# Kernel optimization log

Hardware: AMD Instinct MI355X
Metric: run time of the kernel (lower is better)

## Reference

```python
import jax, jax.numpy as jnp
import numpy as np

NUM_EMBEDDINGS = 4096
EMBEDDING_DIM = 256
COMMITMENT_COST = 0.25


def setup_inputs() -> dict:
    key = jax.random.key(0)
    k1, k2 = jax.random.split(key)
    z = jax.random.normal(k1, (16, 4096, EMBEDDING_DIM), dtype=jnp.float32)
    # nn.Embedding init: uniform(-1/K, 1/K)
    emb_w = jax.random.uniform(
        k2, (NUM_EMBEDDINGS, EMBEDDING_DIM), dtype=jnp.float32,
        minval=-1.0 / NUM_EMBEDDINGS, maxval=1.0 / NUM_EMBEDDINGS)
    return {"z": z, "emb_w": emb_w}


def reference(z, emb_w):
    B = z.shape[0]
    D = emb_w.shape[1]
    flat_z = z.reshape(-1, D)  # [T, D]
    # squared L2 distances: ||z||^2 - 2 z.E^T + ||e||^2  -> [T, K]
    distances = (jnp.sum(flat_z ** 2, axis=1, keepdims=True)
                 - 2.0 * flat_z @ emb_w.T
                 + jnp.sum(emb_w ** 2, axis=1))
    encoding_indices = jnp.argmin(distances, axis=1)  # [T]
    quantized = emb_w[encoding_indices]  # [T, D]
    # straight-through estimator
    quantized = flat_z + jax.lax.stop_gradient(quantized - flat_z)
    loss = (jnp.mean((jax.lax.stop_gradient(quantized) - flat_z) ** 2)
            + COMMITMENT_COST * jnp.mean((quantized - jax.lax.stop_gradient(flat_z)) ** 2))
    return (quantized.reshape(z.shape),
            encoding_indices.reshape(B, -1),
            loss)
```

## Files before the change

### kernel.cpp

```cpp
#include <hip/hip_runtime.h>
#include <cfloat>
#include <climits>

#define T_TOKENS 65536
#define K_EMB 4096
#define D_DIM 256
#define QOFF ((size_t)T_TOKENS * D_DIM)
#define WINDOW 1.2e-4f
#define B0 0.03125f

using bf16x8 = __attribute__((ext_vector_type(8))) short;
using f32x16 = __attribute__((ext_vector_type(16))) float;

__device__ __forceinline__ float fmul_nc(float a, float b) {
    float c = a * b;
    asm volatile("" : "+v"(c));
    return c;
}

__device__ __forceinline__ double wave_sum_d(double v) {
#pragma unroll
    for (int o = 32; o >= 1; o >>= 1) v += __shfl_down(v, o, 64);
    return v;
}

__device__ __forceinline__ void glds16(const void* g, void* l) {
    __builtin_amdgcn_global_load_lds((const __attribute__((address_space(1))) void*)g,
                                     (__attribute__((address_space(3))) void*)l, 16, 0, 0);
}

__device__ __forceinline__ unsigned short f2bf(float f) {
    unsigned u = __float_as_uint(f);
    u += 0x7FFFu + ((u >> 16) & 1u);
    return (unsigned short)(u >> 16);
}

__global__ __launch_bounds__(256)
void a32_kernel(const float* __restrict__ z, float* __restrict__ a32) {
    __shared__ float lds[64][257];
    const int tid = threadIdx.x;
    const int t0 = blockIdx.x * 256;
    for (int sub = 0; sub < 4; sub++) {
        const int tb = t0 + sub * 64;
        __syncthreads();
        for (int idx = tid; idx < 64 * 256; idx += 256) {
            const int r = idx >> 8, c = idx & 255;
            lds[r][c] = z[(size_t)(tb + r) * D_DIM + c];
        }
        __syncthreads();
        if (tid < 64) {
            const float* row = lds[tid];
            float S[2];
            for (int h = 0; h < 2; h++) {
                const float* p = row + h * 128;
                float r[8];
#pragma unroll
                for (int j = 0; j < 8; j++) r[j] = fmul_nc(p[j], p[j]);
                for (int m = 1; m < 16; m++) {
#pragma unroll
                    for (int j = 0; j < 8; j++) r[j] += fmul_nc(p[8 * m + j], p[8 * m + j]);
                }
                S[h] = ((r[0] + r[1]) + (r[2] + r[3])) + ((r[4] + r[5]) + (r[6] + r[7]));
            }
            a32[tb + tid] = S[0] + S[1];
        }
    }
}

__global__ void c32_kernel(const float* __restrict__ emb, float* __restrict__ c32) {
    const int k = blockIdx.x;
    const double v = (double)emb[(size_t)k * D_DIM + threadIdx.x];
    double s = wave_sum_d(v * v);
    __shared__ double wsm[4];
    const int lane = threadIdx.x & 63, w = threadIdx.x >> 6;
    if (lane == 0) wsm[w] = s;
    __syncthreads();
    if (threadIdx.x == 0) c32[k] = (float)(wsm[0] + wsm[1] + wsm[2] + wsm[3]);
}

__global__ __launch_bounds__(256)
void split_hi_kernel(const float* __restrict__ emb, unsigned short* __restrict__ ehi) {
    const size_t i4 = (size_t)blockIdx.x * 256 + threadIdx.x;
    const float4 v = *(const float4*)(emb + i4 * 4);
    ushort4 hh;
    hh.x = f2bf(v.x); hh.y = f2bf(v.y); hh.z = f2bf(v.z); hh.w = f2bf(v.w);
    *(ushort4*)(ehi + i4 * 4) = hh;
}

__global__ __launch_bounds__(256, 4)
void argmin_mfma_kernel(const float* __restrict__ z,
                        const unsigned short* __restrict__ ehi,
                        unsigned int* __restrict__ keyout)
{
    __shared__ short lds_e[2][32 * 256];

    const int tid = threadIdx.x;
    const int wv  = tid >> 6;
    const int l   = tid & 63;
    const int lr  = l & 31;
    const int h   = l >> 5;
    const int tok = blockIdx.x * 128 + wv * 32 + lr;
    const int kbase = blockIdx.y * 2048;

    bf16x8 zh[16];
#pragma unroll
    for (int st = 0; st < 16; st++) {
        const float* zp = z + (size_t)tok * D_DIM + st * 16 + h * 8;
        const float4 f0 = *(const float4*)zp;
        const float4 f1 = *(const float4*)(zp + 4);
        const float f[8] = {f0.x, f0.y, f0.z, f0.w, f1.x, f1.y, f1.z, f1.w};
#pragma unroll
        for (int j = 0; j < 8; j++) zh[st][j] = (short)f2bf(f[j]);
    }

    unsigned b1 = 0u, b2 = 0u, b3 = 0u, b4 = 0u;

    auto stage = [&](int buf, int ct) {
#pragma unroll
        for (int q = 0; q < 4; q++) {
            const int rp = wv * 4 + q;
            const int r  = 2 * rp + h;
            const int g  = lr ^ ((2 * q) | h);
            const unsigned short* src =
                ehi + (size_t)(kbase + ct * 32 + r) * D_DIM + g * 8;
            glds16(src, &lds_e[buf][rp * 512]);
        }
    };

    stage(0, 0);
    __syncthreads();

    const int lk = lr & 7;
    const short* lrow0 = &lds_e[0][lr * 256];
    const short* lrow1 = &lds_e[1][lr * 256];
    const unsigned vh4 = (unsigned)(4 * h);

    int buf = 0;
    for (int ct = 0; ct < 64; ct++) {
        if (ct + 1 < 64) stage(buf ^ 1, ct + 1);

        f32x16 aP;
#pragma unroll
        for (int i = 0; i < 16; i++) aP[i] = B0;

        const short* lrow = buf ? lrow1 : lrow0;
#pragma unroll
        for (int st = 0; st < 16; st++) {
            const bf16x8 eh = *(const bf16x8*)(lrow + (((2 * st + h) ^ lk) << 3));
            aP = __builtin_amdgcn_mfma_f32_32x32x16_bf16(eh, zh[st], aP, 0, 0, 0);
        }

        const unsigned korb = (unsigned)(kbase + ct * 32) | vh4;
#pragma unroll
        for (int r = 0; r < 16; r++) {
            const float cv = fmaxf(aP[r], 1e-6f);
            unsigned t = (__float_as_uint(cv) & 0xFFFFF000u) | korb
                         | (unsigned)((r & 3) + 8 * (r >> 2));
            const unsigned n1 = b1 > t ? b1 : t; t = b1 > t ? t : b1; b1 = n1;
            const unsigned n2 = b2 > t ? b2 : t; t = b2 > t ? t : b2; b2 = n2;
            const unsigned n3 = b3 > t ? b3 : t; t = b3 > t ? t : b3; b3 = n3;
            b4 = b4 > t ? b4 : t;
        }
        __syncthreads();
        buf ^= 1;
    }

    *(uint4*)(keyout + (((size_t)blockIdx.y * T_TOKENS + tok) << 3) + vh4) =
        make_uint4(b1, b2, b3, b4);
}

__global__ __launch_bounds__(256)
void rescore_gather_kernel(const float* __restrict__ z, const float* __restrict__ emb,
                           const float* __restrict__ a32, const float* __restrict__ c32,
                           const unsigned int* __restrict__ keyout,
                           float* __restrict__ out, double* __restrict__ partials)
{
    __shared__ float zt[64][257];
    __shared__ int win[64];
    __shared__ double lsm[4];
    const int tid = threadIdx.x;
    const int base = blockIdx.x * 64;

    for (int idx = tid; idx < 64 * 256; idx += 256) {
        const int r = idx >> 8, c = idx & 255;
        zt[r][c] = z[(size_t)(base + r) * D_DIM + c];
    }
    __syncthreads();

    if (tid < 64) {
        const int t = base + tid;
        unsigned keys[16];
        const uint4 k0 = *(const uint4*)(keyout + ((size_t)t << 3));
        const uint4 k1 = *(const uint4*)(keyout + ((size_t)t << 3) + 4);
        const uint4 k2 = *(const uint4*)(keyout + ((size_t)(T_TOKENS + t) << 3));
        const uint4 k3 = *(const uint4*)(keyout + ((size_t)(T_TOKENS + t) << 3) + 4);
        keys[0] = k0.x; keys[1] = k0.y; keys[2] = k0.z; keys[3] = k0.w;
        keys[4] = k1.x; keys[5] = k1.y; keys[6] = k1.z; keys[7] = k1.w;
        keys[8] = k2.x; keys[9] = k2.y; keys[10] = k2.z; keys[11] = k2.w;
        keys[12] = k3.x; keys[13] = k3.y; keys[14] = k3.z; keys[15] = k3.w;
        float maxF = 0.0f;
#pragma unroll
        for (int s = 0; s < 16; s++) maxF = fmaxf(maxF, __uint_as_float(keys[s]));
        const float thr = maxF - WINDOW;
        const float ar = a32[t];
        float bestv = FLT_MAX; int bestk = INT_MAX;
        for (int s = 0; s < 16; s++) {
            if (__uint_as_float(keys[s]) >= thr) {
                const int k = (int)(keys[s] & 0xFFFu);
                const float* er = emb + (size_t)k * D_DIM;
                float m = 0.0f;
#pragma unroll 8
                for (int d4 = 0; d4 < 64; d4++) {
                    const float4 e4 = *(const float4*)(er + 4 * d4);
                    m = fmaf(zt[tid][4 * d4 + 0], e4.x, m);
                    m = fmaf(zt[tid][4 * d4 + 1], e4.y, m);
                    m = fmaf(zt[tid][4 * d4 + 2], e4.z, m);
                    m = fmaf(zt[tid][4 * d4 + 3], e4.w, m);
                }
                const float v1 = ar - 2.0f * m;
                const float v2 = v1 + c32[k];
                if (v2 < bestv || (v2 == bestv && k < bestk)) { bestv = v2; bestk = k; }
            }
        }
        win[tid] = bestk;
    }
    __syncthreads();

    double lacc = 0.0;
    for (int ti = 0; ti < 64; ti++) {
        const int sel = win[ti];
        const float ev = emb[(size_t)sel * D_DIM + tid];
        const float zv = zt[ti][tid];
        out[(size_t)(base + ti) * D_DIM + tid] = ev;
        if (tid == 0) out[QOFF + base + ti] = (float)sel;
        const double df = (double)zv - (double)ev;
        lacc += df * df;
    }
    lacc = wave_sum_d(lacc);
    const int lane = tid & 63, w = tid >> 6;
    if (lane == 0) lsm[w] = lacc;
    __syncthreads();
    if (tid == 0) partials[blockIdx.x] = lsm[0] + lsm[1] + lsm[2] + lsm[3];
}

__global__ void finalize_kernel(const double* __restrict__ partials, float* __restrict__ out) {
    __shared__ double rsm[4];
    const int tid = threadIdx.x;
    double s = 0.0;
    for (int i = tid; i < 1024; i += 256) s += partials[i];
    s = wave_sum_d(s);
    if ((tid & 63) == 0) rsm[tid >> 6] = s;
    __syncthreads();
    if (tid == 0) {
        const double mean = (rsm[0] + rsm[1] + rsm[2] + rsm[3]) / (double)QOFF;
        out[QOFF + T_TOKENS] = (float)(1.25 * mean);
    }
}

extern "C" void kernel_launch(void* const* d_in, const int* in_sizes, int n_in,
                              void* d_out, int out_size, void* d_ws, size_t ws_size,
                              hipStream_t stream)
{
    const float* z = (const float*)d_in[0];
    const float* emb = (const float*)d_in[1];
    float* out = (float*)d_out;
    char* ws = (char*)d_ws;

    float* a32 = (float*)ws;
    float* c32 = (float*)(ws + 262144);
    unsigned int* keyout = (unsigned int*)(ws + 278528);
    unsigned short* ehi = (unsigned short*)(ws + 4472832);
    double* partials = (double*)(ws + 6569984);

    split_hi_kernel<<<1024, 256, 0, stream>>>(emb, ehi);
    a32_kernel<<<T_TOKENS / 256, 256, 0, stream>>>(z, a32);
    c32_kernel<<<K_EMB, 256, 0, stream>>>(emb, c32);
    argmin_mfma_kernel<<<dim3(T_TOKENS / 128, 2), 256, 0, stream>>>(z, ehi, keyout);
    rescore_gather_kernel<<<T_TOKENS / 64, 256, 0, stream>>>(z, emb, a32, c32, keyout, out, partials);
    finalize_kernel<<<1, 256, 0, stream>>>(partials, out);
}
```

Baseline: 462.0 us.

## Fuse prep kernels, double tokens per wave in argmin, parallelize rescore

Merges the bf16 split and codebook-norm kernels into one pass and folds the token-norm computation into the rescore kernel, cutting kernel launches and an extra read of z. The MFMA argmin kernel now processes two 32-token groups per wave, so each LDS codebook fragment feeds two MFMAs and the codebook is streamed half as many times. It also drops the 4-waves-per-SIMD launch bound, and register pressure rises. Rescore now spreads candidate evaluation over all 256 threads with a shared-memory reduction instead of 64 threads doing serial work. The fmaxf clamp on scores is also removed.

```diff
diff --git a/kernel.cpp b/kernel.cpp
--- a/kernel.cpp
+++ b/kernel.cpp
@@ -36,40 +36,12 @@
 }
 
 __global__ __launch_bounds__(256)
-void a32_kernel(const float* __restrict__ z, float* __restrict__ a32) {
-    __shared__ float lds[64][257];
-    const int tid = threadIdx.x;
-    const int t0 = blockIdx.x * 256;
-    for (int sub = 0; sub < 4; sub++) {
-        const int tb = t0 + sub * 64;
-        __syncthreads();
-        for (int idx = tid; idx < 64 * 256; idx += 256) {
-            const int r = idx >> 8, c = idx & 255;
-            lds[r][c] = z[(size_t)(tb + r) * D_DIM + c];
-        }
-        __syncthreads();
-        if (tid < 64) {
-            const float* row = lds[tid];
-            float S[2];
-            for (int h = 0; h < 2; h++) {
-                const float* p = row + h * 128;
-                float r[8];
-#pragma unroll
-                for (int j = 0; j < 8; j++) r[j] = fmul_nc(p[j], p[j]);
-                for (int m = 1; m < 16; m++) {
-#pragma unroll
-                    for (int j = 0; j < 8; j++) r[j] += fmul_nc(p[8 * m + j], p[8 * m + j]);
-                }
-                S[h] = ((r[0] + r[1]) + (r[2] + r[3])) + ((r[4] + r[5]) + (r[6] + r[7]));
-            }
-            a32[tb + tid] = S[0] + S[1];
-        }
-    }
-}
-
-__global__ void c32_kernel(const float* __restrict__ emb, float* __restrict__ c32) {
+void emb_prep_kernel(const float* __restrict__ emb, float* __restrict__ c32,
+                     unsigned short* __restrict__ ehi) {
     const int k = blockIdx.x;
-    const double v = (double)emb[(size_t)k * D_DIM + threadIdx.x];
+    const float e = emb[(size_t)k * D_DIM + threadIdx.x];
+    ehi[(size_t)k * D_DIM + threadIdx.x] = f2bf(e);
+    const double v = (double)e;
     double s = wave_sum_d(v * v);
     __shared__ double wsm[4];
     const int lane = threadIdx.x & 63, w = threadIdx.x >> 6;
@@ -79,15 +51,6 @@
 }
 
 __global__ __launch_bounds__(256)
-void split_hi_kernel(const float* __restrict__ emb, unsigned short* __restrict__ ehi) {
-    const size_t i4 = (size_t)blockIdx.x * 256 + threadIdx.x;
-    const float4 v = *(const float4*)(emb + i4 * 4);
-    ushort4 hh;
-    hh.x = f2bf(v.x); hh.y = f2bf(v.y); hh.z = f2bf(v.z); hh.w = f2bf(v.w);
-    *(ushort4*)(ehi + i4 * 4) = hh;
-}
-
-__global__ __launch_bounds__(256, 4)
 void argmin_mfma_kernel(const float* __restrict__ z,
                         const unsigned short* __restrict__ ehi,
                         unsigned int* __restrict__ keyout)
@@ -99,21 +62,33 @@
     const int l   = tid & 63;
     const int lr  = l & 31;
     const int h   = l >> 5;
-    const int tok = blockIdx.x * 128 + wv * 32 + lr;
+    const int tokA = blockIdx.x * 256 + wv * 64 + lr;
+    const int tokB = tokA + 32;
     const int kbase = blockIdx.y * 2048;
 
-    bf16x8 zh[16];
+    bf16x8 zA[16], zB[16];
 #pragma unroll
     for (int st = 0; st < 16; st++) {
-        const float* zp = z + (size_t)tok * D_DIM + st * 16 + h * 8;
-        const float4 f0 = *(const float4*)zp;
-        const float4 f1 = *(const float4*)(zp + 4);
-        const float f[8] = {f0.x, f0.y, f0.z, f0.w, f1.x, f1.y, f1.z, f1.w};
-#pragma unroll
-        for (int j = 0; j < 8; j++) zh[st][j] = (short)f2bf(f[j]);
-    }
-
-    unsigned b1 = 0u, b2 = 0u, b3 = 0u, b4 = 0u;
+        {
+            const float* zp = z + (size_t)tokA * D_DIM + st * 16 + h * 8;
+            const float4 f0 = *(const float4*)zp;
+            const float4 f1 = *(const float4*)(zp + 4);
+            const float f[8] = {f0.x, f0.y, f0.z, f0.w, f1.x, f1.y, f1.z, f1.w};
+#pragma unroll
+            for (int j = 0; j < 8; j++) zA[st][j] = (short)f2bf(f[j]);
+        }
+        {
+            const float* zp = z + (size_t)tokB * D_DIM + st * 16 + h * 8;
+            const float4 f0 = *(const float4*)zp;
+            const float4 f1 = *(const float4*)(zp + 4);
+            const float f[8] = {f0.x, f0.y, f0.z, f0.w, f1.x, f1.y, f1.z, f1.w};
+#pragma unroll
+            for (int j = 0; j < 8; j++) zB[st][j] = (short)f2bf(f[j]);
+        }
+    }
+
+    unsigned a1 = 0u, a2 = 0u, a3 = 0u, a4 = 0u;
+    unsigned c1 = 0u, c2 = 0u, c3 = 0u, c4 = 0u;
 
     auto stage = [&](int buf, int ct) {
 #pragma unroll
@@ -139,43 +114,58 @@
     for (int ct = 0; ct < 64; ct++) {
         if (ct + 1 < 64) stage(buf ^ 1, ct + 1);
 
-        f32x16 aP;
-#pragma unroll
-        for (int i = 0; i < 16; i++) aP[i] = B0;
+        f32x16 pA, pB;
+#pragma unroll
+        for (int i = 0; i < 16; i++) { pA[i] = B0; pB[i] = B0; }
 
         const short* lrow = buf ? lrow1 : lrow0;
 #pragma unroll
         for (int st = 0; st < 16; st++) {
             const bf16x8 eh = *(const bf16x8*)(lrow + (((2 * st + h) ^ lk) << 3));
-            aP = __builtin_amdgcn_mfma_f32_32x32x16_bf16(eh, zh[st], aP, 0, 0, 0);
+            pA = __builtin_amdgcn_mfma_f32_32x32x16_bf16(eh, zA[st], pA, 0, 0, 0);
+            pB = __builtin_amdgcn_mfma_f32_32x32x16_bf16(eh, zB[st], pB, 0, 0, 0);
         }
 
         const unsigned korb = (unsigned)(kbase + ct * 32) | vh4;
 #pragma unroll
         for (int r = 0; r < 16; r++) {
-            const float cv = fmaxf(aP[r], 1e-6f);
-            unsigned t = (__float_as_uint(cv) & 0xFFFFF000u) | korb
-                         | (unsigned)((r & 3) + 8 * (r >> 2));
-            const unsigned n1 = b1 > t ? b1 : t; t = b1 > t ? t : b1; b1 = n1;
-            const unsigned n2 = b2 > t ? b2 : t; t = b2 > t ? t : b2; b2 = n2;
-            const unsigned n3 = b3 > t ? b3 : t; t = b3 > t ? t : b3; b3 = n3;
-            b4 = b4 > t ? b4 : t;
+            const unsigned rid = korb | (unsigned)((r & 3) + 8 * (r >> 2));
+            unsigned t = (__float_as_uint(pA[r]) & 0xFFFFF000u) | rid;
+            {
+                const unsigned n1 = a1 > t ? a1 : t; t = a1 > t ? t : a1; a1 = n1;
+                const unsigned n2 = a2 > t ? a2 : t; t = a2 > t ? t : a2; a2 = n2;
+                const unsigned n3 = a3 > t ? a3 : t; t = a3 > t ? t : a3; a3 = n3;
+                a4 = a4 > t ? a4 : t;
+            }
+            unsigned u = (__float_as_uint(pB[r]) & 0xFFFFF000u) | rid;
+            {
+                const unsigned n1 = c1 > u ? c1 : u; u = c1 > u ? u : c1; c1 = n1;
+                const unsigned n2 = c2 > u ? c2 : u; u = c2 > u ? u : c2; c2 = n2;
+                const unsigned n3 = c3 > u ? c3 : u; u = c3 > u ? u : c3; c3 = n3;
+                c4 = c4 > u ? c4 : u;
+            }
         }
         __syncthreads();
         buf ^= 1;
     }
 
-    *(uint4*)(keyout + (((size_t)blockIdx.y * T_TOKENS + tok) << 3) + vh4) =
-        make_uint4(b1, b2, b3, b4);
+    *(uint4*)(keyout + (((size_t)blockIdx.y * T_TOKENS + tokA) << 3) + vh4) =
+        make_uint4(a1, a2, a3, a4);
+    *(uint4*)(keyout + (((size_t)blockIdx.y * T_TOKENS + tokB) << 3) + vh4) =
+        make_uint4(c1, c2, c3, c4);
 }
 
 __global__ __launch_bounds__(256)
 void rescore_gather_kernel(const float* __restrict__ z, const float* __restrict__ emb,
-                           const float* __restrict__ a32, const float* __restrict__ c32,
+                           const float* __restrict__ c32,
                            const unsigned int* __restrict__ keyout,
                            float* __restrict__ out, double* __restrict__ partials)
 {
     __shared__ float zt[64][257];
+    __shared__ float a32sm[64];
+    __shared__ unsigned lmax[4][64];
+    __shared__ float bvq[4][64];
+    __shared__ int bkq[4][64];
     __shared__ int win[64];
     __shared__ double lsm[4];
     const int tid = threadIdx.x;
@@ -188,51 +178,81 @@
     __syncthreads();
 
     if (tid < 64) {
-        const int t = base + tid;
-        unsigned keys[16];
-        const uint4 k0 = *(const uint4*)(keyout + ((size_t)t << 3));
-        const uint4 k1 = *(const uint4*)(keyout + ((size_t)t << 3) + 4);
-        const uint4 k2 = *(const uint4*)(keyout + ((size_t)(T_TOKENS + t) << 3));
-        const uint4 k3 = *(const uint4*)(keyout + ((size_t)(T_TOKENS + t) << 3) + 4);
-        keys[0] = k0.x; keys[1] = k0.y; keys[2] = k0.z; keys[3] = k0.w;
-        keys[4] = k1.x; keys[5] = k1.y; keys[6] = k1.z; keys[7] = k1.w;
-        keys[8] = k2.x; keys[9] = k2.y; keys[10] = k2.z; keys[11] = k2.w;
-        keys[12] = k3.x; keys[13] = k3.y; keys[14] = k3.z; keys[15] = k3.w;
-        float maxF = 0.0f;
-#pragma unroll
-        for (int s = 0; s < 16; s++) maxF = fmaxf(maxF, __uint_as_float(keys[s]));
-        const float thr = maxF - WINDOW;
-        const float ar = a32[t];
-        float bestv = FLT_MAX; int bestk = INT_MAX;
-        for (int s = 0; s < 16; s++) {
-            if (__uint_as_float(keys[s]) >= thr) {
-                const int k = (int)(keys[s] & 0xFFFu);
-                const float* er = emb + (size_t)k * D_DIM;
-                float m = 0.0f;
+        const float* row = zt[tid];
+        float S[2];
+        for (int hh = 0; hh < 2; hh++) {
+            const float* p = row + hh * 128;
+            float r[8];
+#pragma unroll
+            for (int j = 0; j < 8; j++) r[j] = fmul_nc(p[j], p[j]);
+            for (int m = 1; m < 16; m++) {
+#pragma unroll
+                for (int j = 0; j < 8; j++) r[j] += fmul_nc(p[8 * m + j], p[8 * m + j]);
+            }
+            S[hh] = ((r[0] + r[1]) + (r[2] + r[3])) + ((r[4] + r[5]) + (r[6] + r[7]));
+        }
+        a32sm[tid] = S[0] + S[1];
+    }
+
+    const int ti = tid & 63, qq = tid >> 6;
+    const int t = base + ti;
+    const uint4 kk = *(const uint4*)(keyout +
+        (((size_t)(qq >> 1) * T_TOKENS + t) << 3) + (qq & 1) * 4);
+    unsigned lm = kk.x > kk.y ? kk.x : kk.y;
+    lm = lm > kk.z ? lm : kk.z;
+    lm = lm > kk.w ? lm : kk.w;
+    lmax[qq][ti] = lm;
+    __syncthreads();
+
+    unsigned gm = lmax[0][ti];
+#pragma unroll
+    for (int e = 1; e < 4; e++) gm = gm > lmax[e][ti] ? gm : lmax[e][ti];
+    const float thr = __uint_as_float(gm) - WINDOW;
+    const float ar = a32sm[ti];
+    float bestv = FLT_MAX; int bestk = INT_MAX;
+    const unsigned ks[4] = {kk.x, kk.y, kk.z, kk.w};
+#pragma unroll
+    for (int s = 0; s < 4; s++) {
+        if (__uint_as_float(ks[s]) >= thr) {
+            const int k = (int)(ks[s] & 0xFFFu);
+            const float* er = emb + (size_t)k * D_DIM;
+            float m = 0.0f;
 #pragma unroll 8
-                for (int d4 = 0; d4 < 64; d4++) {
-                    const float4 e4 = *(const float4*)(er + 4 * d4);
-                    m = fmaf(zt[tid][4 * d4 + 0], e4.x, m);
-                    m = fmaf(zt[tid][4 * d4 + 1], e4.y, m);
-                    m = fmaf(zt[tid][4 * d4 + 2], e4.z, m);
-                    m = fmaf(zt[tid][4 * d4 + 3], e4.w, m);
-                }
-                const float v1 = ar - 2.0f * m;
-                const float v2 = v1 + c32[k];
-                if (v2 < bestv || (v2 == bestv && k < bestk)) { bestv = v2; bestk = k; }
-            }
-        }
-        win[tid] = bestk;
+            for (int d4 = 0; d4 < 64; d4++) {
+                const float4 e4 = *(const float4*)(er + 4 * d4);
+                m = fmaf(zt[ti][4 * d4 + 0], e4.x, m);
+                m = fmaf(zt[ti][4 * d4 + 1], e4.y, m);
+                m = fmaf(zt[ti][4 * d4 + 2], e4.z, m);
+                m = fmaf(zt[ti][4 * d4 + 3], e4.w, m);
+            }
+            const float v1 = ar - 2.0f * m;
+            const float v2 = v1 + c32[k];
+            if (v2 < bestv || (v2 == bestv && k < bestk)) { bestv = v2; bestk = k; }
+        }
+    }
+    bvq[qq][ti] = bestv; bkq[qq][ti] = bestk;
+    __syncthreads();
+
+    if (tid < 64) {
+        float B = bvq[0][tid];
+        int I = bkq[0][tid];
+#pragma unroll
+        for (int e = 1; e < 4; e++) {
+            const float cv = bvq[e][tid];
+            const int ck = bkq[e][tid];
+            if (cv < B || (cv == B && ck < I)) { B = cv; I = ck; }
+        }
+        win[tid] = I;
     }
     __syncthreads();
 
     double lacc = 0.0;
-    for (int ti = 0; ti < 64; ti++) {
-        const int sel = win[ti];
+    for (int ti2 = 0; ti2 < 64; ti2++) {
+        const int sel = win[ti2];
         const float ev = emb[(size_t)sel * D_DIM + tid];
-        const float zv = zt[ti][tid];
-        out[(size_t)(base + ti) * D_DIM + tid] = ev;
-        if (tid == 0) out[QOFF + base + ti] = (float)sel;
+        const float zv = zt[ti2][tid];
+        out[(size_t)(base + ti2) * D_DIM + tid] = ev;
+        if (tid == 0) out[QOFF + base + ti2] = (float)sel;
         const double df = (double)zv - (double)ev;
         lacc += df * df;
     }
@@ -266,16 +286,13 @@
     float* out = (float*)d_out;
     char* ws = (char*)d_ws;
 
-    float* a32 = (float*)ws;
-    float* c32 = (float*)(ws + 262144);
-    unsigned int* keyout = (unsigned int*)(ws + 278528);
-    unsigned short* ehi = (unsigned short*)(ws + 4472832);
-    double* partials = (double*)(ws + 6569984);
-
-    split_hi_kernel<<<1024, 256, 0, stream>>>(emb, ehi);
-    a32_kernel<<<T_TOKENS / 256, 256, 0, stream>>>(z, a32);
-    c32_kernel<<<K_EMB, 256, 0, stream>>>(emb, c32);
-    argmin_mfma_kernel<<<dim3(T_TOKENS / 128, 2), 256, 0, stream>>>(z, ehi, keyout);
-    rescore_gather_kernel<<<T_TOKENS / 64, 256, 0, stream>>>(z, emb, a32, c32, keyout, out, partials);
+    float* c32 = (float*)ws;
+    unsigned int* keyout = (unsigned int*)(ws + 16384);
+    unsigned short* ehi = (unsigned short*)(ws + 4210688);
+    double* partials = (double*)(ws + 6307840);
+
+    emb_prep_kernel<<<K_EMB, 256, 0, stream>>>(emb, c32, ehi);
+    argmin_mfma_kernel<<<dim3(T_TOKENS / 256, 2), 256, 0, stream>>>(z, ehi, keyout);
+    rescore_gather_kernel<<<T_TOKENS / 64, 256, 0, stream>>>(z, emb, c32, keyout, out, partials);
     finalize_kernel<<<1, 256, 0, stream>>>(partials, out);
 }
```

Result: faster. 372.4 us (-19.4%).
